# Kernel tuning notes

Measured on AMD Instinct MI355X. Metric: run time of the kernel, lower is better.

## Reference

```python
import jax, jax.numpy as jnp
import numpy as np

SOM_H, SOM_W, LATENT = 8, 8, 64


def setup_inputs() -> dict:
    key = jax.random.key(0)
    ks = jax.random.split(key, 5)
    B, D = 32768, 2048
    return {
        "x": jax.random.normal(ks[0], (B, D), dtype=jnp.float32),
        "W_enc": jax.random.normal(ks[1], (D, LATENT), dtype=jnp.float32) * 0.02,
        "b_enc": jnp.zeros((LATENT,), dtype=jnp.float32),
        "W_dec_q": jax.random.normal(ks[2], (LATENT, D), dtype=jnp.float32) * 0.02,
        "b_dec_q": jnp.zeros((D,), dtype=jnp.float32),
        "W_dec_e": jax.random.normal(ks[3], (LATENT, D), dtype=jnp.float32) * 0.02,
        "b_dec_e": jnp.zeros((D,), dtype=jnp.float32),
        "embeddings": jax.random.normal(ks[4], (SOM_H, SOM_W, LATENT), dtype=jnp.float32) * 0.05,
    }


def reference(x, W_enc, b_enc, W_dec_q, b_dec_q, W_dec_e, b_dec_e, embeddings):
    # encoder: [B, D] -> [B, L]
    z_e = x @ W_enc + b_enc
    # squared distances to all SOM codes, expanded form (same math as sum((z-e)^2))
    E = embeddings.reshape(SOM_H * SOM_W, LATENT)                 # [64, L]
    z_dist_flat = (
        jnp.sum(z_e * z_e, axis=-1, keepdims=True)
        - 2.0 * (z_e @ E.T)
        + jnp.sum(E * E, axis=-1)
    )                                                             # [B, 64]
    k = jnp.argmin(z_dist_flat, axis=-1)                          # [B]
    k_1 = k // SOM_W
    k_2 = k % SOM_W
    z_q = embeddings[k_1, k_2]                                    # [B, L]

    k1_not_top = k_1 < SOM_H - 1
    k1_not_bottom = k_1 > 0
    k2_not_left = k_2 > 0
    k1_up = jnp.where(k1_not_top, k_1 + 1, k_1)
    k1_down = jnp.where(k1_not_bottom, k_1 - 1, k_1)
    k2_left = jnp.where(k2_not_left, k_2 - 1, k_2)

    zero = jnp.zeros_like(z_q)
    z_q_up = jnp.where(k1_not_top[:, None], embeddings[k1_up, k_2], zero)
    z_q_down = jnp.where(k1_not_bottom[:, None], embeddings[k1_down, k_2], zero)
    # NOTE: original torch code uses `==` instead of `=` for the right neighbor,
    # so z_q_right stays all-zeros. Replicated faithfully.
    z_q_right = zero
    z_q_left = jnp.where(k2_not_left[:, None], embeddings[k_1, k2_left], zero)

    z_q_neighbors = jnp.stack([z_q, z_q_up, z_q_down, z_q_right, z_q_left], axis=1)  # [B,5,L]

    x_q = z_q @ W_dec_q + b_dec_q
    x_e = z_e @ W_dec_e + b_dec_e
    return (x_e, x_q, z_e, z_q, z_q_neighbors, k, z_dist_flat)
```

## Files before the change

kernel.cpp:

```cpp
#include <hip/hip_runtime.h>
#include <stdint.h>

constexpr size_t OFF_XQ = (size_t)32768 * 2048;
constexpr size_t OFF_ZE = OFF_XQ * 2;
constexpr size_t OFF_ZQ = OFF_ZE + (size_t)32768 * 64;
constexpr size_t OFF_NB = OFF_ZQ + (size_t)32768 * 64;
constexpr size_t OFF_K  = OFF_NB + (size_t)32768 * 5 * 64;
constexpr size_t OFF_ZD = OFF_K + 32768;

typedef __attribute__((ext_vector_type(8))) short short8;
typedef __attribute__((ext_vector_type(4))) float f32x4;
typedef __attribute__((ext_vector_type(4))) unsigned short us4;

__device__ __forceinline__ unsigned short f2bf(float f) {
  unsigned int u = __float_as_uint(f);
  u += 0x7fffu + ((u >> 16) & 1u);
  return (unsigned short)(u >> 16);
}

__device__ __forceinline__ float pick4(float4 v, int c) {
  float r = v.x;
  r = (c == 1) ? v.y : r;
  r = (c == 2) ? v.z : r;
  r = (c == 3) ? v.w : r;
  return r;
}

__global__ __launch_bounds__(256) void somvae_wprep(
    const float* __restrict__ We, const float* __restrict__ Wq,
    unsigned short* __restrict__ wt)
{
  const int sel = blockIdx.y;
  const float* W = sel ? Wq : We;
  unsigned short* WT = wt + (size_t)sel * (64 * 2048);
  const int d0 = blockIdx.x * 64;
  __shared__ unsigned short tl[64][68];
  const int t = threadIdx.x;
  for (int i = 4 * t; i < 4096; i += 1024) {
    int l = i >> 6, dd = i & 63;
    float4 v = *(const float4*)(W + (size_t)l * 2048 + d0 + dd);
    tl[dd + 0][l] = f2bf(v.x);
    tl[dd + 1][l] = f2bf(v.y);
    tl[dd + 2][l] = f2bf(v.z);
    tl[dd + 3][l] = f2bf(v.w);
  }
  __syncthreads();
  {
    int dd = t >> 2, c4 = (t & 3) * 16;
    #pragma unroll
    for (int q = 0; q < 4; ++q) {
      us4 v;
      v.x = tl[dd][c4 + 4 * q + 0];
      v.y = tl[dd][c4 + 4 * q + 1];
      v.z = tl[dd][c4 + 4 * q + 2];
      v.w = tl[dd][c4 + 4 * q + 3];
      *(us4*)(WT + (size_t)(d0 + dd) * 64 + c4 + 4 * q) = v;
    }
  }
}

__global__ __launch_bounds__(256, 2) void somvae_encoder(
    const float* __restrict__ x, const float* __restrict__ W_enc,
    const float* __restrict__ b_enc, const float* __restrict__ emb,
    float* __restrict__ out)
{
  __shared__ float xsT[64][68];
  __shared__ float ws[64][68];
  __shared__ float Erow[64][68];
  __shared__ double eeD[64];

  const int t   = threadIdx.x;
  const int tx  = t & 15;
  const int ty  = t >> 4;
  const int row0 = blockIdx.x * 64;

  for (int i = 4 * t; i < 4096; i += 1024) {
    float4 v = *(const float4*)(emb + i);
    int c = i >> 6, j = i & 63;
    *(float4*)&Erow[c][j] = v;
  }
  __syncthreads();
  if (t < 64) {
    double s = 0.0;
    #pragma unroll
    for (int j = 0; j < 64; ++j) { double v = (double)Erow[t][j]; s += v * v; }
    eeD[t] = s;
  }

  float acc[4][4] = {};
  for (int kb = 0; kb < 2048; kb += 64) {
    __syncthreads();
    {
      const int m = t & 15, r = t >> 4;
      #pragma unroll
      for (int p = 0; p < 4; ++p) {
        const int rr = r + p * 16;
        float4 v = *(const float4*)(x + (size_t)(row0 + rr) * 2048 + kb + m * 4);
        #pragma unroll
        for (int c0 = 0; c0 < 4; ++c0) {
          int c = (c0 + m) & 3;
          xsT[m * 4 + c][rr] = pick4(v, c);
        }
        float4 wv = *(const float4*)(W_enc + (size_t)(kb + rr) * 64 + m * 4);
        *(float4*)&ws[rr][m * 4] = wv;
      }
    }
    __syncthreads();
    #pragma unroll 8
    for (int k = 0; k < 64; ++k) {
      float4 a = *(const float4*)&xsT[k][ty * 4];
      float4 b = *(const float4*)&ws[k][tx * 4];
      float av[4] = {a.x, a.y, a.z, a.w};
      float bv[4] = {b.x, b.y, b.z, b.w};
      #pragma unroll
      for (int i = 0; i < 4; ++i)
        #pragma unroll
        for (int j = 0; j < 4; ++j)
          acc[i][j] = fmaf(av[i], bv[j], acc[i][j]);
    }
  }

  __syncthreads();
  float (*zs)[68] = xsT;
  {
    float4 be = *(const float4*)(b_enc + tx * 4);
    float bb[4] = {be.x, be.y, be.z, be.w};
    #pragma unroll
    for (int i = 0; i < 4; ++i) {
      const int r = ty * 4 + i;
      float4 v = make_float4(acc[i][0] + bb[0], acc[i][1] + bb[1],
                             acc[i][2] + bb[2], acc[i][3] + bb[3]);
      *(float4*)(out + OFF_ZE + (size_t)(row0 + r) * 64 + tx * 4) = v;
      *(float4*)&zs[r][tx * 4] = v;
    }
  }
  __syncthreads();

  {
    const int lane = t & 63;
    const int rbase = (t >> 6) * 16;
    for (int rr = 0; rr < 16; ++rr) {
      const int r = rbase + rr;
      float dotf = 0.f, sf = 0.f;
      #pragma unroll
      for (int j4 = 0; j4 < 64; j4 += 4) {
        float4 z4 = *(const float4*)&zs[r][j4];
        float4 e4 = *(const float4*)&Erow[lane][j4];
        dotf = fmaf(z4.x, e4.x, dotf); dotf = fmaf(z4.y, e4.y, dotf);
        dotf = fmaf(z4.z, e4.z, dotf); dotf = fmaf(z4.w, e4.w, dotf);
        sf = fmaf(z4.x, z4.x, sf); sf = fmaf(z4.y, z4.y, sf);
        sf = fmaf(z4.z, z4.z, sf); sf = fmaf(z4.w, z4.w, sf);
      }
      double d = (double)sf - 2.0 * (double)dotf + eeD[lane];
      double bd = d; int bi = lane;
      #pragma unroll
      for (int off = 32; off; off >>= 1) {
        double od = __shfl_xor(bd, off, 64);
        int    oi = __shfl_xor(bi, off, 64);
        if (od < bd || (od == bd && oi < bi)) { bd = od; bi = oi; }
      }
      const int k  = bi;
      const int k1 = k >> 3, k2 = k & 7;
      const size_t row = (size_t)(row0 + r);
      const int kup = (k1 < 7) ? k + 8 : k;
      const int kdn = (k1 > 0) ? k - 8 : k;
      const int klf = (k2 > 0) ? k - 1 : k;
      float zq = Erow[k][lane];
      out[OFF_ZQ + row * 64 + lane] = zq;
      const size_t nb = OFF_NB + row * 320;
      out[nb +   0 + lane] = zq;
      out[nb +  64 + lane] = (k1 < 7) ? Erow[kup][lane] : 0.f;
      out[nb + 128 + lane] = (k1 > 0) ? Erow[kdn][lane] : 0.f;
      out[nb + 192 + lane] = 0.f;
      out[nb + 256 + lane] = (k2 > 0) ? Erow[klf][lane] : 0.f;
      out[OFF_ZD + row * 64 + lane] = (float)d;
      if (lane == 0) out[OFF_K + row] = (float)k;
    }
  }
}

__global__ __launch_bounds__(256) void somvae_decoder(
    const float* __restrict__ Wq, const float* __restrict__ bq,
    const float* __restrict__ We, const float* __restrict__ be,
    const unsigned short* __restrict__ wt, int use_wt,
    float* __restrict__ out)
{
  const int sel = blockIdx.y;
  const float* bias = sel ? bq : be;
  const float* Wf   = sel ? Wq : We;
  const unsigned short* WT = wt + (size_t)sel * (64 * 2048);
  const float* z = out + (sel ? OFF_ZQ : OFF_ZE);
  float* xo = out + (sel ? OFF_XQ : (size_t)0);
  const int row0 = blockIdx.x * 64;

  const int t = threadIdx.x;
  const int lane = t & 63, w = t >> 6;
  const int m = lane & 15, quad = lane >> 4;

  short8 a0, a1;
  {
    const float* zp = z + (size_t)(row0 + 16 * w + m) * 64 + quad * 8;
    float4 u0 = *(const float4*)(zp);
    float4 u1 = *(const float4*)(zp + 4);
    float4 u2 = *(const float4*)(zp + 32);
    float4 u3 = *(const float4*)(zp + 36);
    a0[0]=(short)f2bf(u0.x); a0[1]=(short)f2bf(u0.y); a0[2]=(short)f2bf(u0.z); a0[3]=(short)f2bf(u0.w);
    a0[4]=(short)f2bf(u1.x); a0[5]=(short)f2bf(u1.y); a0[6]=(short)f2bf(u1.z); a0[7]=(short)f2bf(u1.w);
    a1[0]=(short)f2bf(u2.x); a1[1]=(short)f2bf(u2.y); a1[2]=(short)f2bf(u2.z); a1[3]=(short)f2bf(u2.w);
    a1[4]=(short)f2bf(u3.x); a1[5]=(short)f2bf(u3.y); a1[6]=(short)f2bf(u3.z); a1[7]=(short)f2bf(u3.w);
  }

  for (int ct = 0; ct < 32; ++ct) {
    const int d0 = ct * 64;
    #pragma unroll
    for (int c = 0; c < 4; ++c) {
      const int d = d0 + 16 * c + m;
      short8 b0, b1;
      if (use_wt) {
        const unsigned short* wp = WT + (size_t)d * 64;
        b0 = *(const short8*)(wp + quad * 8);
        b1 = *(const short8*)(wp + 32 + quad * 8);
      } else {
        #pragma unroll
        for (int j = 0; j < 8; ++j) {
          b0[j] = (short)f2bf(Wf[(size_t)(quad * 8 + j) * 2048 + d]);
          b1[j] = (short)f2bf(Wf[(size_t)(32 + quad * 8 + j) * 2048 + d]);
        }
      }
      f32x4 acc = {0.f, 0.f, 0.f, 0.f};
      acc = __builtin_amdgcn_mfma_f32_16x16x32_bf16(a0, b0, acc, 0, 0, 0);
      acc = __builtin_amdgcn_mfma_f32_16x16x32_bf16(a1, b1, acc, 0, 0, 0);
      const float bv = bias[d];
      float* op = xo + (size_t)(row0 + 16 * w + quad * 4) * 2048 + d;
      op[0]        = acc[0] + bv;
      op[2048]     = acc[1] + bv;
      op[2 * 2048] = acc[2] + bv;
      op[3 * 2048] = acc[3] + bv;
    }
  }
}

extern "C" void kernel_launch(void* const* d_in, const int* in_sizes, int n_in,
                              void* d_out, int out_size, void* d_ws, size_t ws_size,
                              hipStream_t stream) {
  (void)in_sizes; (void)n_in; (void)out_size;
  const float* x       = (const float*)d_in[0];
  const float* W_enc   = (const float*)d_in[1];
  const float* b_enc   = (const float*)d_in[2];
  const float* W_dec_q = (const float*)d_in[3];
  const float* b_dec_q = (const float*)d_in[4];
  const float* W_dec_e = (const float*)d_in[5];
  const float* b_dec_e = (const float*)d_in[6];
  const float* emb     = (const float*)d_in[7];
  float* out = (float*)d_out;
  unsigned short* wt = (unsigned short*)d_ws;
  const int use_wt = (ws_size >= (size_t)2 * 64 * 2048 * sizeof(unsigned short)) ? 1 : 0;

  if (use_wt)
    somvae_wprep<<<dim3(32, 2), 256, 0, stream>>>(W_dec_e, W_dec_q, wt);
  somvae_encoder<<<dim3(512), 256, 0, stream>>>(x, W_enc, b_enc, emb, out);
  somvae_decoder<<<dim3(512, 2), 256, 0, stream>>>(W_dec_q, b_dec_q, W_dec_e, b_dec_e,
                                                   wt, use_wt, out);
}
```

Before: 1.068 ms.

## Fuse encoder, SOM assignment and both decoders into one kernel

Merges the encoder and decoder kernels into one. z_e and z_q stay in shared memory and are fed to MFMA decoding directly, so they are no longer re-read from global memory and a launch is dropped. The encoder GEMM is reworked to load x row-major without a transpose, with a K-split across two thread groups that is reduced through shared memory. The decoder MFMA operands are swapped so each thread writes float4 outputs along D, replacing scalar strided stores. The cost is that the encoder grid of 512 blocks now also does all decoder work, which limits parallelism during the write-heavy decode phase.

```diff
diff --git a/kernel.cpp b/kernel.cpp
--- a/kernel.cpp
+++ b/kernel.cpp
@@ -16,14 +16,6 @@
   unsigned int u = __float_as_uint(f);
   u += 0x7fffu + ((u >> 16) & 1u);
   return (unsigned short)(u >> 16);
-}
-
-__device__ __forceinline__ float pick4(float4 v, int c) {
-  float r = v.x;
-  r = (c == 1) ? v.y : r;
-  r = (c == 2) ? v.z : r;
-  r = (c == 3) ? v.w : r;
-  return r;
 }
 
 __global__ __launch_bounds__(256) void somvae_wprep(
@@ -59,25 +51,26 @@
   }
 }
 
-__global__ __launch_bounds__(256, 2) void somvae_encoder(
+__global__ __launch_bounds__(256, 2) void somvae_fused(
     const float* __restrict__ x, const float* __restrict__ W_enc,
     const float* __restrict__ b_enc, const float* __restrict__ emb,
+    const float* __restrict__ Wq, const float* __restrict__ bq,
+    const float* __restrict__ We, const float* __restrict__ be,
+    const unsigned short* __restrict__ wt, int use_wt,
     float* __restrict__ out)
 {
-  __shared__ float xsT[64][68];
+  __shared__ float xs[64][68];
   __shared__ float ws[64][68];
   __shared__ float Erow[64][68];
   __shared__ double eeD[64];
-
-  const int t   = threadIdx.x;
-  const int tx  = t & 15;
-  const int ty  = t >> 4;
+  __shared__ int kidxs[64];
+
+  const int t = threadIdx.x;
   const int row0 = blockIdx.x * 64;
 
   for (int i = 4 * t; i < 4096; i += 1024) {
     float4 v = *(const float4*)(emb + i);
-    int c = i >> 6, j = i & 63;
-    *(float4*)&Erow[c][j] = v;
+    *(float4*)&Erow[i >> 6][i & 63] = v;
   }
   __syncthreads();
   if (t < 64) {
@@ -87,69 +80,81 @@
     eeD[t] = s;
   }
 
-  float acc[4][4] = {};
+  const int kg = t >> 7;
+  const int ty = (t >> 4) & 7;
+  const int tx = t & 15;
+  const int srow = t >> 2;
+  const int scol = (t & 3) * 16;
+
+  float acc[8][4] = {};
   for (int kb = 0; kb < 2048; kb += 64) {
     __syncthreads();
-    {
-      const int m = t & 15, r = t >> 4;
-      #pragma unroll
-      for (int p = 0; p < 4; ++p) {
-        const int rr = r + p * 16;
-        float4 v = *(const float4*)(x + (size_t)(row0 + rr) * 2048 + kb + m * 4);
+    #pragma unroll
+    for (int q = 0; q < 4; ++q) {
+      *(float4*)&xs[srow][scol + 4 * q] =
+          *(const float4*)(x + (size_t)(row0 + srow) * 2048 + kb + scol + 4 * q);
+      *(float4*)&ws[srow][scol + 4 * q] =
+          *(const float4*)(W_enc + (size_t)(kb + srow) * 64 + scol + 4 * q);
+    }
+    __syncthreads();
+    const int k0 = kg * 32;
+    #pragma unroll
+    for (int kq = 0; kq < 8; ++kq) {
+      const int kbq = k0 + 4 * kq;
+      f32x4 wv[4];
+      #pragma unroll
+      for (int kk = 0; kk < 4; ++kk)
+        wv[kk] = *(const f32x4*)&ws[kbq + kk][4 * tx];
+      #pragma unroll
+      for (int i = 0; i < 8; ++i) {
+        f32x4 a = *(const f32x4*)&xs[ty + 8 * i][kbq];
         #pragma unroll
-        for (int c0 = 0; c0 < 4; ++c0) {
-          int c = (c0 + m) & 3;
-          xsT[m * 4 + c][rr] = pick4(v, c);
-        }
-        float4 wv = *(const float4*)(W_enc + (size_t)(kb + rr) * 64 + m * 4);
-        *(float4*)&ws[rr][m * 4] = wv;
-      }
-    }
-    __syncthreads();
-    #pragma unroll 8
-    for (int k = 0; k < 64; ++k) {
-      float4 a = *(const float4*)&xsT[k][ty * 4];
-      float4 b = *(const float4*)&ws[k][tx * 4];
-      float av[4] = {a.x, a.y, a.z, a.w};
-      float bv[4] = {b.x, b.y, b.z, b.w};
-      #pragma unroll
-      for (int i = 0; i < 4; ++i)
-        #pragma unroll
-        for (int j = 0; j < 4; ++j)
-          acc[i][j] = fmaf(av[i], bv[j], acc[i][j]);
-    }
-  }
-
-  __syncthreads();
-  float (*zs)[68] = xsT;
+        for (int kk = 0; kk < 4; ++kk)
+          #pragma unroll
+          for (int j = 0; j < 4; ++j)
+            acc[i][j] = fmaf(a[kk], wv[kk][j], acc[i][j]);
+      }
+    }
+  }
+
+  __syncthreads();
+  float (*zs)[68] = ws;
+  if (kg == 1) {
+    #pragma unroll
+    for (int i = 0; i < 8; ++i) {
+      f32x4 av = {acc[i][0], acc[i][1], acc[i][2], acc[i][3]};
+      *(f32x4*)&zs[ty + 8 * i][4 * tx] = av;
+    }
+  }
+  __syncthreads();
+  if (kg == 0) {
+    f32x4 be4 = *(const f32x4*)(b_enc + 4 * tx);
+    #pragma unroll
+    for (int i = 0; i < 8; ++i) {
+      const int r = ty + 8 * i;
+      f32x4 v = *(const f32x4*)&zs[r][4 * tx];
+      #pragma unroll
+      for (int j = 0; j < 4; ++j) v[j] = v[j] + acc[i][j] + be4[j];
+      *(f32x4*)&zs[r][4 * tx] = v;
+      *(f32x4*)(out + OFF_ZE + (size_t)(row0 + r) * 64 + 4 * tx) = v;
+    }
+  }
+  __syncthreads();
+
+  const int lane = t & 63;
   {
-    float4 be = *(const float4*)(b_enc + tx * 4);
-    float bb[4] = {be.x, be.y, be.z, be.w};
-    #pragma unroll
-    for (int i = 0; i < 4; ++i) {
-      const int r = ty * 4 + i;
-      float4 v = make_float4(acc[i][0] + bb[0], acc[i][1] + bb[1],
-                             acc[i][2] + bb[2], acc[i][3] + bb[3]);
-      *(float4*)(out + OFF_ZE + (size_t)(row0 + r) * 64 + tx * 4) = v;
-      *(float4*)&zs[r][tx * 4] = v;
-    }
-  }
-  __syncthreads();
-
-  {
-    const int lane = t & 63;
     const int rbase = (t >> 6) * 16;
     for (int rr = 0; rr < 16; ++rr) {
       const int r = rbase + rr;
       float dotf = 0.f, sf = 0.f;
       #pragma unroll
       for (int j4 = 0; j4 < 64; j4 += 4) {
-        float4 z4 = *(const float4*)&zs[r][j4];
-        float4 e4 = *(const float4*)&Erow[lane][j4];
-        dotf = fmaf(z4.x, e4.x, dotf); dotf = fmaf(z4.y, e4.y, dotf);
-        dotf = fmaf(z4.z, e4.z, dotf); dotf = fmaf(z4.w, e4.w, dotf);
-        sf = fmaf(z4.x, z4.x, sf); sf = fmaf(z4.y, z4.y, sf);
-        sf = fmaf(z4.z, z4.z, sf); sf = fmaf(z4.w, z4.w, sf);
+        f32x4 z4 = *(const f32x4*)&zs[r][j4];
+        f32x4 e4 = *(const f32x4*)&Erow[lane][j4];
+        dotf = fmaf(z4[0], e4[0], dotf); dotf = fmaf(z4[1], e4[1], dotf);
+        dotf = fmaf(z4[2], e4[2], dotf); dotf = fmaf(z4[3], e4[3], dotf);
+        sf = fmaf(z4[0], z4[0], sf); sf = fmaf(z4[1], z4[1], sf);
+        sf = fmaf(z4[2], z4[2], sf); sf = fmaf(z4[3], z4[3], sf);
       }
       double d = (double)sf - 2.0 * (double)dotf + eeD[lane];
       double bd = d; int bi = lane;
@@ -174,68 +179,63 @@
       out[nb + 192 + lane] = 0.f;
       out[nb + 256 + lane] = (k2 > 0) ? Erow[klf][lane] : 0.f;
       out[OFF_ZD + row * 64 + lane] = (float)d;
-      if (lane == 0) out[OFF_K + row] = (float)k;
-    }
-  }
-}
-
-__global__ __launch_bounds__(256) void somvae_decoder(
-    const float* __restrict__ Wq, const float* __restrict__ bq,
-    const float* __restrict__ We, const float* __restrict__ be,
-    const unsigned short* __restrict__ wt, int use_wt,
-    float* __restrict__ out)
-{
-  const int sel = blockIdx.y;
-  const float* bias = sel ? bq : be;
-  const float* Wf   = sel ? Wq : We;
-  const unsigned short* WT = wt + (size_t)sel * (64 * 2048);
-  const float* z = out + (sel ? OFF_ZQ : OFF_ZE);
-  float* xo = out + (sel ? OFF_XQ : (size_t)0);
-  const int row0 = blockIdx.x * 64;
-
-  const int t = threadIdx.x;
-  const int lane = t & 63, w = t >> 6;
-  const int m = lane & 15, quad = lane >> 4;
-
-  short8 a0, a1;
+      if (lane == 0) { out[OFF_K + row] = (float)k; kidxs[r] = k; }
+    }
+  }
+  __syncthreads();
+
   {
-    const float* zp = z + (size_t)(row0 + 16 * w + m) * 64 + quad * 8;
-    float4 u0 = *(const float4*)(zp);
-    float4 u1 = *(const float4*)(zp + 4);
-    float4 u2 = *(const float4*)(zp + 32);
-    float4 u3 = *(const float4*)(zp + 36);
-    a0[0]=(short)f2bf(u0.x); a0[1]=(short)f2bf(u0.y); a0[2]=(short)f2bf(u0.z); a0[3]=(short)f2bf(u0.w);
-    a0[4]=(short)f2bf(u1.x); a0[5]=(short)f2bf(u1.y); a0[6]=(short)f2bf(u1.z); a0[7]=(short)f2bf(u1.w);
-    a1[0]=(short)f2bf(u2.x); a1[1]=(short)f2bf(u2.y); a1[2]=(short)f2bf(u2.z); a1[3]=(short)f2bf(u2.w);
-    a1[4]=(short)f2bf(u3.x); a1[5]=(short)f2bf(u3.y); a1[6]=(short)f2bf(u3.z); a1[7]=(short)f2bf(u3.w);
-  }
-
-  for (int ct = 0; ct < 32; ++ct) {
-    const int d0 = ct * 64;
-    #pragma unroll
-    for (int c = 0; c < 4; ++c) {
-      const int d = d0 + 16 * c + m;
-      short8 b0, b1;
-      if (use_wt) {
-        const unsigned short* wp = WT + (size_t)d * 64;
-        b0 = *(const short8*)(wp + quad * 8);
-        b1 = *(const short8*)(wp + 32 + quad * 8);
-      } else {
+    const int w = t >> 6;
+    const int m = lane & 15, quad = lane >> 4;
+    for (int sel = 0; sel < 2; ++sel) {
+      const float* bias = sel ? bq : be;
+      const float* Wf   = sel ? Wq : We;
+      const unsigned short* WTs = wt + (size_t)sel * (64 * 2048);
+      float* xo = out + (sel ? OFF_XQ : (size_t)0);
+
+      short8 bz[4][2];
+      #pragma unroll
+      for (int rg = 0; rg < 4; ++rg) {
+        const int br = rg * 16 + m;
+        const float* zp = sel ? &Erow[kidxs[br]][0] : &zs[br][0];
         #pragma unroll
-        for (int j = 0; j < 8; ++j) {
-          b0[j] = (short)f2bf(Wf[(size_t)(quad * 8 + j) * 2048 + d]);
-          b1[j] = (short)f2bf(Wf[(size_t)(32 + quad * 8 + j) * 2048 + d]);
+        for (int h = 0; h < 2; ++h) {
+          f32x4 u0 = *(const f32x4*)(zp + 32 * h + quad * 8);
+          f32x4 u1 = *(const f32x4*)(zp + 32 * h + quad * 8 + 4);
+          short8 b;
+          b[0] = (short)f2bf(u0[0]); b[1] = (short)f2bf(u0[1]);
+          b[2] = (short)f2bf(u0[2]); b[3] = (short)f2bf(u0[3]);
+          b[4] = (short)f2bf(u1[0]); b[5] = (short)f2bf(u1[1]);
+          b[6] = (short)f2bf(u1[2]); b[7] = (short)f2bf(u1[3]);
+          bz[rg][h] = b;
         }
       }
-      f32x4 acc = {0.f, 0.f, 0.f, 0.f};
-      acc = __builtin_amdgcn_mfma_f32_16x16x32_bf16(a0, b0, acc, 0, 0, 0);
-      acc = __builtin_amdgcn_mfma_f32_16x16x32_bf16(a1, b1, acc, 0, 0, 0);
-      const float bv = bias[d];
-      float* op = xo + (size_t)(row0 + 16 * w + quad * 4) * 2048 + d;
-      op[0]        = acc[0] + bv;
-      op[2048]     = acc[1] + bv;
-      op[2 * 2048] = acc[2] + bv;
-      op[3 * 2048] = acc[3] + bv;
+
+      for (int dt = w; dt < 128; dt += 4) {
+        const int d0 = dt * 16;
+        short8 a0, a1;
+        if (use_wt) {
+          const unsigned short* wp = WTs + (size_t)(d0 + m) * 64 + quad * 8;
+          a0 = *(const short8*)(wp);
+          a1 = *(const short8*)(wp + 32);
+        } else {
+          #pragma unroll
+          for (int j = 0; j < 8; ++j) {
+            a0[j] = (short)f2bf(Wf[(size_t)(quad * 8 + j) * 2048 + d0 + m]);
+            a1[j] = (short)f2bf(Wf[(size_t)(32 + quad * 8 + j) * 2048 + d0 + m]);
+          }
+        }
+        f32x4 bv = *(const f32x4*)(bias + d0 + quad * 4);
+        #pragma unroll
+        for (int rg = 0; rg < 4; ++rg) {
+          f32x4 acc2 = {0.f, 0.f, 0.f, 0.f};
+          acc2 = __builtin_amdgcn_mfma_f32_16x16x32_bf16(a0, bz[rg][0], acc2, 0, 0, 0);
+          acc2 = __builtin_amdgcn_mfma_f32_16x16x32_bf16(a1, bz[rg][1], acc2, 0, 0, 0);
+          #pragma unroll
+          for (int j = 0; j < 4; ++j) acc2[j] += bv[j];
+          *(f32x4*)(xo + (size_t)(row0 + rg * 16 + m) * 2048 + d0 + quad * 4) = acc2;
+        }
+      }
     }
   }
 }
@@ -258,7 +258,7 @@
 
   if (use_wt)
     somvae_wprep<<<dim3(32, 2), 256, 0, stream>>>(W_dec_e, W_dec_q, wt);
-  somvae_encoder<<<dim3(512), 256, 0, stream>>>(x, W_enc, b_enc, emb, out);
-  somvae_decoder<<<dim3(512, 2), 256, 0, stream>>>(W_dec_q, b_dec_q, W_dec_e, b_dec_e,
-                                                   wt, use_wt, out);
-}
+  somvae_fused<<<dim3(512), 256, 0, stream>>>(x, W_enc, b_enc, emb,
+                                              W_dec_q, b_dec_q, W_dec_e, b_dec_e,
+                                              wt, use_wt, out);
+}
```

New measurement: 932.2 us. -12.7%, faster.
